# Performance work log

Hardware: AMD Instinct MI355X
Metric: run time of the kernel (lower is better)

## Reference

```python
import jax, jax.numpy as jnp
import numpy as np

EMBED_DIM = 1024
NUM_HEADS = 16
HEAD_DIM = EMBED_DIM // NUM_HEADS
EPS = 1e-5


def setup_inputs() -> dict:
    key = jax.random.key(0)
    ks = jax.random.split(key, 7)
    B, S, D = 4, 2048, EMBED_DIM
    s = 1.0 / np.sqrt(D)
    return {
        "x": jax.random.normal(ks[0], (B, S, D), dtype=jnp.float32),
        "W_qkv": jax.random.uniform(ks[1], (D, 3 * D), jnp.float32, -s, s),
        "b_qkv": jax.random.uniform(ks[2], (3 * D,), jnp.float32, -s, s),
        "W_out": jax.random.uniform(ks[3], (D, D), jnp.float32, -s, s),
        "b_out": jax.random.uniform(ks[4], (D,), jnp.float32, -s, s),
        "gamma": jnp.ones((D,), jnp.float32),
        "beta": jnp.zeros((D,), jnp.float32),
    }


def _layer_norm(y, gamma, beta):
    mu = jnp.mean(y, axis=-1, keepdims=True)
    var = jnp.mean(jnp.square(y - mu), axis=-1, keepdims=True)
    return (y - mu) * jax.lax.rsqrt(var + EPS) * gamma + beta


def reference(x, W_qkv, b_qkv, W_out, b_out, gamma, beta):
    B, S, D = x.shape
    H, Hd = NUM_HEADS, HEAD_DIM
    qkv = x @ W_qkv + b_qkv                       # [B,S,3D]
    q, k, v = jnp.split(qkv, 3, axis=-1)
    q = q.reshape(B, S, H, Hd).transpose(0, 2, 1, 3)  # [B,H,S,Hd]
    k = k.reshape(B, S, H, Hd).transpose(0, 2, 1, 3)
    v = v.reshape(B, S, H, Hd).transpose(0, 2, 1, 3)
    scale = 1.0 / np.sqrt(Hd)
    scores = jnp.einsum("bhsd,bhtd->bhst", q, k) * scale  # [B,H,S,S]
    attn = jax.nn.softmax(scores, axis=-1)
    ctx = jnp.einsum("bhst,bhtd->bhsd", attn, v)  # [B,H,S,Hd]
    ctx = ctx.transpose(0, 2, 1, 3).reshape(B, S, D)
    out = ctx @ W_out + b_out
    return _layer_norm(out + x, gamma, beta)
```

## Files before the change

### kernel.cpp

```cpp
#include <hip/hip_runtime.h>
#include <stdint.h>
#include <stddef.h>


#define SEQ    2048
#define DMODEL 1024
#define NHEAD  16
#define HDIM   64

typedef __attribute__((ext_vector_type(4))) float f32x4;
typedef __attribute__((ext_vector_type(16))) float f32x16;
typedef __attribute__((ext_vector_type(8))) short bf16x8;
typedef __attribute__((ext_vector_type(2))) unsigned uint2v;

static __device__ __forceinline__ unsigned short f2b(float f) {
  union { float f; unsigned u; } c; c.f = f;
  unsigned r = c.u + 0x7FFFu + ((c.u >> 16) & 1u);
  return (unsigned short)(r >> 16);
}
static __device__ __forceinline__ unsigned pkbf(float lo, float hi_) {
  unsigned r;
  asm("v_cvt_pk_bf16_f32 %0, %1, %2" : "=v"(r) : "v"(lo), "v"(hi_));
  return r;
}
static __device__ __forceinline__ float exp2v(float x) {
  return __builtin_amdgcn_exp2f(x);
}
static __device__ __forceinline__ uint2v swap32(unsigned a, unsigned b) {
  return __builtin_amdgcn_permlane32_swap(a, b, false, false);
}
static __device__ __forceinline__ void gl_lds16(const void* g, void* l) {
  __builtin_amdgcn_global_load_lds((const __attribute__((address_space(1))) void*)g,
                                   (__attribute__((address_space(3))) void*)l, 16, 0, 0);
}
static __device__ __forceinline__ int swz(int row, int col) {
  return (row * 64 + col) ^ ((row & 7) << 3);
}

__global__ __launch_bounds__(256) void k_prep(const float* __restrict__ Wqkv,
                                              const float* __restrict__ Wout,
                                              const float* __restrict__ X,
                                              unsigned short* __restrict__ wqkvT,
                                              unsigned short* __restrict__ woutT,
                                              unsigned short* __restrict__ Xb) {
  __shared__ unsigned short tile[32][33];
  const int bid = blockIdx.x;
  const int t = threadIdx.x;
  if (bid < 4096) {
    const float* in; unsigned short* out; int C, bx, by;
    if (bid < 3072) { in = Wqkv; out = wqkvT; C = 3072; bx = bid % 96; by = bid / 96; }
    else { int b2 = bid - 3072; in = Wout; out = woutT; C = 1024; bx = b2 & 31; by = b2 >> 5; }
    const int R = 1024;
    const int c0 = bx * 32, r0 = by * 32;
    const int tx = t & 31, ty = t >> 5;
#pragma unroll
    for (int j = 0; j < 4; j++) {
      int rr = ty + j * 8;
      tile[rr][tx] = f2b(in[(size_t)(r0 + rr) * C + c0 + tx]);
    }
    __syncthreads();
#pragma unroll
    for (int j = 0; j < 4; j++) {
      int rr = ty + j * 8;
      out[(size_t)(c0 + rr) * R + r0 + tx] = tile[tx][rr];
    }
  } else {
    const size_t i = ((size_t)(bid - 4096) * 256 + t) * 8;
    f32x4 a = *(const f32x4*)&X[i];
    f32x4 b = *(const f32x4*)&X[i + 4];
    bf16x8 o;
    o[0] = (short)f2b(a[0]); o[1] = (short)f2b(a[1]);
    o[2] = (short)f2b(a[2]); o[3] = (short)f2b(a[3]);
    o[4] = (short)f2b(b[0]); o[5] = (short)f2b(b[1]);
    o[6] = (short)f2b(b[2]); o[7] = (short)f2b(b[3]);
    *(bf16x8*)&Xb[i] = o;
  }
}

__global__ __launch_bounds__(256) void k_gemm_qkv(const unsigned short* __restrict__ X,
                                                  const unsigned short* __restrict__ WT,
                                                  const float* __restrict__ bias,
                                                  unsigned short* __restrict__ qb,
                                                  unsigned short* __restrict__ kb,
                                                  unsigned short* __restrict__ vt) {
  __shared__ __align__(16) unsigned short As[128 * 32];
  __shared__ __align__(16) unsigned short Bs[128 * 32];
  const int t = threadIdx.x;
  const int w = t >> 6, l = t & 63, g = l >> 4, r = l & 15;
  const int wr = w >> 1, wc = w & 1;
  const int bm = blockIdx.x * 128;
  const int bn = blockIdx.y * 128;

  f32x4 acc[4][4];
#pragma unroll
  for (int a = 0; a < 4; a++)
#pragma unroll
    for (int b = 0; b < 4; b++) acc[a][b] = f32x4{0.f, 0.f, 0.f, 0.f};

  for (int k0 = 0; k0 < DMODEL; k0 += 32) {
    __syncthreads();
#pragma unroll
    for (int j = 0; j < 2; j++) {
      int idx = t + j * 256;
      int row = idx >> 2, kc = idx & 3;
      gl_lds16(X + (size_t)(bm + row) * DMODEL + k0 + kc * 8, (char*)As + idx * 16);
      gl_lds16(WT + (size_t)(bn + row) * DMODEL + k0 + kc * 8, (char*)Bs + idx * 16);
    }
    __syncthreads();
    bf16x8 af[4], bf[4];
#pragma unroll
    for (int mf = 0; mf < 4; mf++)
      af[mf] = *(const bf16x8*)&As[(wr * 64 + mf * 16 + r) * 32 + g * 8];
#pragma unroll
    for (int nf = 0; nf < 4; nf++)
      bf[nf] = *(const bf16x8*)&Bs[(wc * 64 + nf * 16 + r) * 32 + g * 8];
#pragma unroll
    for (int mf = 0; mf < 4; mf++)
#pragma unroll
      for (int nf = 0; nf < 4; nf++)
        acc[mf][nf] = __builtin_amdgcn_mfma_f32_16x16x32_bf16(af[mf], bf[nf], acc[mf][nf], 0, 0, 0);
  }

  if (blockIdx.y >= 16) {
    __syncthreads();
    const int bi = bm >> 11, sbase = bm & 2047;
    const int h  = ((bn - 2048) >> 6) + wc;
    const int bh = bi * NHEAD + h;
    unsigned short* Ls = (w < 2) ? (As + w * 2048) : (Bs + (w - 2) * 2048);
#pragma unroll
    for (int p = 0; p < 2; p++) {
#pragma unroll
      for (int nfp = 0; nfp < 2; nfp++)
#pragma unroll
        for (int mf = 0; mf < 4; mf++)
#pragma unroll
          for (int i = 0; i < 4; i++) {
            const int nf = 2 * p + nfp;
            const int dd = nfp * 16 + r;
            const int ss = mf * 16 + g * 4 + i;
            float v = acc[mf][nf][i] + bias[bn + wc * 64 + nf * 16 + r];
            Ls[dd * 64 + (((ss >> 3) ^ (dd & 7)) * 8) + (ss & 7)] = f2b(v);
          }
#pragma unroll
      for (int j = 0; j < 4; j++) {
        const int dd = l >> 1;
        const int ch = (l & 1) * 4 + j;
        bf16x8 ov = *(const bf16x8*)&Ls[dd * 64 + ((ch ^ (dd & 7)) * 8)];
        *(bf16x8*)&vt[((size_t)bh * HDIM + 32 * p + dd) * SEQ + sbase + wr * 64 + ch * 8] = ov;
      }
    }
  } else {
#pragma unroll
    for (int mf = 0; mf < 4; mf++)
#pragma unroll
      for (int nf = 0; nf < 4; nf++)
#pragma unroll
        for (int i = 0; i < 4; i++) {
          int m = bm + wr * 64 + mf * 16 + g * 4 + i;
          int n = bn + wc * 64 + nf * 16 + r;
          float v = acc[mf][nf][i] + bias[n];
          int part = n >> 10, rem = n & 1023, h = rem >> 6, d = rem & 63;
          int bi = m >> 11, s = m & 2047;
          int bh = bi * NHEAD + h;
          if (part == 0)      qb[((size_t)bh * SEQ + s) * HDIM + d] = f2b(v * 0.18033688f);
          else                kb[((size_t)bh * SEQ + s) * HDIM + d] = f2b(v);
        }
  }
}

__global__ __launch_bounds__(512) void k_attn(const unsigned short* __restrict__ qb,
                                              const unsigned short* __restrict__ kb,
                                              const unsigned short* __restrict__ vt,
                                              unsigned short* __restrict__ ctx) {
  __shared__ __align__(16) unsigned short Qs[256 * 64];
  __shared__ __align__(16) unsigned short K0[64 * 64];
  __shared__ __align__(16) unsigned short K1[64 * 64];
  __shared__ __align__(16) unsigned short V0[64 * 64];
  __shared__ __align__(16) unsigned short V1[64 * 64];
  const int t = threadIdx.x;
  const int w = t >> 6, l = t & 63;
  const int ql = l & 31, hi = l >> 5;
  const int bid = blockIdx.x;
  const int xcd = bid & 7;
  const int j_  = bid >> 3;
  const int bh  = xcd * 8 + (j_ >> 3);
  const int q0  = (j_ & 7) * 256;
  const size_t qoff = ((size_t)bh * SEQ + q0) * HDIM;

#pragma unroll
  for (int j = 0; j < 4; j++) {
    int idx = t + j * 512;
    int row = idx >> 3, s = idx & 7;
    gl_lds16(qb + qoff + (size_t)row * 64 + (s ^ (row & 7)) * 8, (char*)Qs + idx * 16);
  }
  {
    int row = t >> 3, s = t & 7;
    gl_lds16(kb + ((size_t)bh * SEQ + row) * HDIM + (s ^ (row & 7)) * 8, (char*)K0 + t * 16);
    gl_lds16(vt + ((size_t)bh * HDIM + row) * SEQ + (s ^ (row & 7)) * 8, (char*)V0 + t * 16);
  }
  asm volatile("s_waitcnt vmcnt(2)" ::: "memory");
  __builtin_amdgcn_sched_barrier(0);
  __builtin_amdgcn_s_barrier();

  bf16x8 qf[4];
#pragma unroll
  for (int ds = 0; ds < 4; ds++)
    qf[ds] = *(const bf16x8*)&Qs[swz(w * 32 + ql, ds * 16 + hi * 8)];
  asm volatile("s_waitcnt lgkmcnt(0)" ::: "memory");

  bf16x8 ones;
#pragma unroll
  for (int i = 0; i < 8; i++) ones[i] = (short)0x3F80;

  f32x16 acc_o[2];
  f32x16 acc_l;
#pragma unroll
  for (int db = 0; db < 2; db++)
#pragma unroll
    for (int i = 0; i < 16; i++) acc_o[db][i] = 0.f;
#pragma unroll
  for (int i = 0; i < 16; i++) acc_l[i] = 0.f;

  for (int it = 0; it < SEQ / 64; ++it) {
    const int b = it & 1;
    if (it + 1 < SEQ / 64) {
      const int kt = (it + 1) * 64;
      unsigned short* Kd = b ? K0 : K1;
      unsigned short* Vd = b ? V0 : V1;
      {
        int row = t >> 3, s = t & 7;
        gl_lds16(kb + ((size_t)bh * SEQ + kt + row) * HDIM + (s ^ (row & 7)) * 8,
                 (char*)Kd + t * 16);
        gl_lds16(vt + ((size_t)bh * HDIM + row) * SEQ + kt + (s ^ (row & 7)) * 8,
                 (char*)Vd + t * 16);
      }
      asm volatile("s_waitcnt vmcnt(2)" ::: "memory");
    } else {
      asm volatile("s_waitcnt vmcnt(0)" ::: "memory");
    }
    __builtin_amdgcn_sched_barrier(0);
    __builtin_amdgcn_s_barrier();

    const unsigned short* Kb = b ? K1 : K0;
    const unsigned short* Vb = b ? V1 : V0;

    bf16x8 kf[2][4];
#pragma unroll
    for (int kb2 = 0; kb2 < 2; kb2++)
#pragma unroll
      for (int ds = 0; ds < 4; ds++)
        kf[kb2][ds] = *(const bf16x8*)&Kb[swz(kb2 * 32 + ql, ds * 16 + hi * 8)];

    f32x16 accs[2];
#pragma unroll
    for (int kb2 = 0; kb2 < 2; kb2++)
#pragma unroll
      for (int i = 0; i < 16; i++) accs[kb2][i] = 0.f;
    __builtin_amdgcn_s_setprio(1);
#pragma unroll
    for (int ds = 0; ds < 4; ds++)
#pragma unroll
      for (int kb2 = 0; kb2 < 2; kb2++)
        accs[kb2] = __builtin_amdgcn_mfma_f32_32x32x16_bf16(kf[kb2][ds], qf[ds], accs[kb2], 0, 0, 0);
    __builtin_amdgcn_s_setprio(0);

#pragma unroll
    for (int kb2 = 0; kb2 < 2; kb2++)
#pragma unroll
      for (int i = 0; i < 16; i++) accs[kb2][i] = exp2v(accs[kb2][i]);

    bf16x8 pa[4];
#pragma unroll
    for (int ks = 0; ks < 4; ks++) {
      const int kb2 = ks >> 1, rb = (ks & 1) * 8;
      unsigned wA0 = pkbf(accs[kb2][rb + 0], accs[kb2][rb + 1]);
      unsigned wA1 = pkbf(accs[kb2][rb + 2], accs[kb2][rb + 3]);
      unsigned wB0 = pkbf(accs[kb2][rb + 4], accs[kb2][rb + 5]);
      unsigned wB1 = pkbf(accs[kb2][rb + 6], accs[kb2][rb + 7]);
      uint2v s0 = swap32(wB0, wA0);
      uint2v s1 = swap32(wB1, wA1);
      union { bf16x8 v; unsigned u[4]; } fr;
      fr.u[0] = s0[1]; fr.u[1] = s1[1]; fr.u[2] = s0[0]; fr.u[3] = s1[0];
      pa[ks] = fr.v;
    }

    bf16x8 vf[2][4];
#pragma unroll
    for (int db = 0; db < 2; db++)
#pragma unroll
      for (int ks = 0; ks < 4; ks++)
        vf[db][ks] = *(const bf16x8*)&Vb[swz(db * 32 + ql, ks * 16 + hi * 8)];

    __builtin_amdgcn_s_setprio(1);
#pragma unroll
    for (int ks = 0; ks < 4; ks++) {
#pragma unroll
      for (int db = 0; db < 2; db++)
        acc_o[db] = __builtin_amdgcn_mfma_f32_32x32x16_bf16(vf[db][ks], pa[ks], acc_o[db], 0, 0, 0);
      acc_l = __builtin_amdgcn_mfma_f32_32x32x16_bf16(ones, pa[ks], acc_l, 0, 0, 0);
    }
    __builtin_amdgcn_s_setprio(0);

    __builtin_amdgcn_s_barrier();
  }

  const int bi = bh >> 4, h = bh & 15;
  const float rl = 1.f / acc_l[0];
  unsigned short* Ls = Qs + w * 2048;
#pragma unroll
  for (int db = 0; db < 2; db++)
#pragma unroll
    for (int j = 0; j < 8; j++) {
      const int d0 = db * 32 + (j & 1) * 2 + (j >> 1) * 8 + hi * 4;
      *(unsigned*)&Ls[(ql * 64 + d0) ^ ((ql & 7) << 3)] =
          pkbf(acc_o[db][2 * j] * rl, acc_o[db][2 * j + 1] * rl);
    }
#pragma unroll
  for (int rq = 0; rq < 4; rq++) {
    const int q = rq * 8 + (l >> 3);
    const int c8 = l & 7;
    bf16x8 ov = *(const bf16x8*)&Ls[(q * 64 + c8 * 8) ^ ((q & 7) << 3)];
    *(bf16x8*)&ctx[((size_t)bi * SEQ + q0 + w * 32 + q) * DMODEL + h * 64 + c8 * 8] = ov;
  }
}

__global__ __launch_bounds__(256) void k_gemm_out(const unsigned short* __restrict__ A,
                                                  const unsigned short* __restrict__ WT,
                                                  const float* __restrict__ bias,
                                                  const float* __restrict__ X,
                                                  float* __restrict__ Y) {
  __shared__ __align__(16) unsigned short As[128 * 32];
  __shared__ __align__(16) unsigned short Bs[128 * 32];
  const int t = threadIdx.x;
  const int w = t >> 6, l = t & 63, g = l >> 4, r = l & 15;
  const int wr = w >> 1, wc = w & 1;
  const int bm = blockIdx.x * 128;
  const int bn = blockIdx.y * 128;

  f32x4 acc[4][4];
#pragma unroll
  for (int a = 0; a < 4; a++)
#pragma unroll
    for (int b = 0; b < 4; b++) acc[a][b] = f32x4{0.f, 0.f, 0.f, 0.f};

  for (int k0 = 0; k0 < DMODEL; k0 += 32) {
    __syncthreads();
#pragma unroll
    for (int j = 0; j < 2; j++) {
      int idx = t + j * 256;
      int row = idx >> 2, kc = idx & 3;
      gl_lds16(A + (size_t)(bm + row) * DMODEL + k0 + kc * 8, (char*)As + idx * 16);
      gl_lds16(WT + (size_t)(bn + row) * DMODEL + k0 + kc * 8, (char*)Bs + idx * 16);
    }
    __syncthreads();
    bf16x8 af[4], bf[4];
#pragma unroll
    for (int mf = 0; mf < 4; mf++)
      af[mf] = *(const bf16x8*)&As[(wr * 64 + mf * 16 + r) * 32 + g * 8];
#pragma unroll
    for (int nf = 0; nf < 4; nf++)
      bf[nf] = *(const bf16x8*)&Bs[(wc * 64 + nf * 16 + r) * 32 + g * 8];
#pragma unroll
    for (int mf = 0; mf < 4; mf++)
#pragma unroll
      for (int nf = 0; nf < 4; nf++)
        acc[mf][nf] = __builtin_amdgcn_mfma_f32_16x16x32_bf16(af[mf], bf[nf], acc[mf][nf], 0, 0, 0);
  }

#pragma unroll
  for (int mf = 0; mf < 4; mf++)
#pragma unroll
    for (int nf = 0; nf < 4; nf++)
#pragma unroll
      for (int i = 0; i < 4; i++) {
        int m = bm + wr * 64 + mf * 16 + g * 4 + i;
        int n = bn + wc * 64 + nf * 16 + r;
        float v = acc[mf][nf][i] + bias[n] + X[(size_t)m * DMODEL + n];
        Y[(size_t)m * DMODEL + n] = v;
      }
}

__global__ __launch_bounds__(256) void k_ln(const float* __restrict__ Y,
                                            const float* __restrict__ gamma,
                                            const float* __restrict__ beta,
                                            float* __restrict__ out) {
  const int row = blockIdx.x, t = threadIdx.x;
  const float* y = Y + (size_t)row * DMODEL;
  f32x4 v = *(const f32x4*)&y[t * 4];
  float s = v[0] + v[1] + v[2] + v[3];
  float q = v[0] * v[0] + v[1] * v[1] + v[2] * v[2] + v[3] * v[3];
#pragma unroll
  for (int m = 1; m < 64; m <<= 1) { s += __shfl_xor(s, m); q += __shfl_xor(q, m); }
  __shared__ float ss[4], sq[4];
  const int w = t >> 6, l = t & 63;
  if (l == 0) { ss[w] = s; sq[w] = q; }
  __syncthreads();
  s = ss[0] + ss[1] + ss[2] + ss[3];
  q = sq[0] + sq[1] + sq[2] + sq[3];
  const float mu = s * (1.f / DMODEL);
  const float var = q * (1.f / DMODEL) - mu * mu;
  const float rs = rsqrtf(var + 1e-5f);
  f32x4 o;
#pragma unroll
  for (int j = 0; j < 4; j++)
    o[j] = (v[j] - mu) * rs * gamma[t * 4 + j] + beta[t * 4 + j];
  *(f32x4*)&out[(size_t)row * DMODEL + t * 4] = o;
}

extern "C" void kernel_launch(void* const* d_in, const int* in_sizes, int n_in,
                              void* d_out, int out_size, void* d_ws, size_t ws_size,
                              hipStream_t stream) {
  const float* X     = (const float*)d_in[0];
  const float* Wqkv  = (const float*)d_in[1];
  const float* bqkv  = (const float*)d_in[2];
  const float* Wout  = (const float*)d_in[3];
  const float* bout  = (const float*)d_in[4];
  const float* gamma = (const float*)d_in[5];
  const float* beta  = (const float*)d_in[6];

  char* ws = (char*)d_ws;
  unsigned short* wqkvT = (unsigned short*)(ws);
  unsigned short* woutT = (unsigned short*)(ws + 6291456);
  unsigned short* Xb    = (unsigned short*)(ws + 8388608);
  unsigned short* ctx   = (unsigned short*)(ws + 8388608);
  unsigned short* qb    = (unsigned short*)(ws + 25165824);
  unsigned short* kb    = (unsigned short*)(ws + 41943040);
  unsigned short* vt    = (unsigned short*)(ws + 58720256);
  float*          Yf    = (float*)d_out;

  k_prep<<<dim3(8192, 1, 1), dim3(256, 1, 1), 0, stream>>>(Wqkv, Wout, X, wqkvT, woutT, Xb);
  k_gemm_qkv<<<dim3(64, 24, 1), dim3(256, 1, 1), 0, stream>>>(Xb, wqkvT, bqkv, qb, kb, vt);
  k_attn<<<dim3(512, 1, 1), dim3(512, 1, 1), 0, stream>>>(qb, kb, vt, ctx);
  k_gemm_out<<<dim3(64, 8, 1), dim3(256, 1, 1), 0, stream>>>(ctx, woutT, bout, X, Yf);
  k_ln<<<dim3(8192, 1, 1), dim3(256, 1, 1), 0, stream>>>(Yf, gamma, beta, (float*)d_out);
}
```

Measured before the change: 208.5 us.

## Software-pipeline QK^T one tile ahead and replace ones-MFMA row sum with lane reduction

Restructures the attention loop so the QK^T MFMAs for the next key tile are issued before the exp/pack/PV work of the current tile, with K loaded two tiles ahead and V one tile ahead. Scores alternate between two accumulator sets across a manually unrolled pair of iterations. The softmax denominator is now a register sum plus a permlane32 swap instead of an extra MFMA against a ones vector. This removes a quarter of the PV MFMA work and overlaps matrix and transcendental work, at the cost of more live registers and fp32 rather than bf16-rounded denominators.

New measurement: 209.5 us. Within noise of the previous version (+0.5%).

```diff
diff --git a/kernel.cpp b/kernel.cpp
--- a/kernel.cpp
+++ b/kernel.cpp
@@ -28,6 +28,12 @@
 }
 static __device__ __forceinline__ uint2v swap32(unsigned a, unsigned b) {
   return __builtin_amdgcn_permlane32_swap(a, b, false, false);
+}
+static __device__ __forceinline__ float xchg_sum(float v) {
+  union { float f; unsigned u; } c; c.f = v;
+  uint2v p = swap32(c.u, c.u);
+  union { unsigned u; float f; } x, y; x.u = p[0]; y.u = p[1];
+  return x.f + y.f;
 }
 static __device__ __forceinline__ void gl_lds16(const void* g, void* l) {
   __builtin_amdgcn_global_load_lds((const __attribute__((address_space(1))) void*)g,
@@ -165,6 +171,82 @@
           if (part == 0)      qb[((size_t)bh * SEQ + s) * HDIM + d] = f2b(v * 0.18033688f);
           else                kb[((size_t)bh * SEQ + s) * HDIM + d] = f2b(v);
         }
+  }
+}
+
+static __device__ __forceinline__ void attn_iter(
+    int it, int t, int ql, int hi, int bh,
+    const unsigned short* __restrict__ kb, const unsigned short* __restrict__ vt,
+    unsigned short* K0, unsigned short* K1, unsigned short* V0, unsigned short* V1,
+    const bf16x8 (&qf)[4], f32x16 (&cur)[2], f32x16 (&nxt)[2],
+    f32x16 (&acc_o)[2], float& l_run) {
+  asm volatile("s_waitcnt vmcnt(0)" ::: "memory");
+  __builtin_amdgcn_sched_barrier(0);
+  __builtin_amdgcn_s_barrier();
+  if (it + 2 < SEQ / 64) {
+    int row = t >> 3, s = t & 7;
+    gl_lds16(kb + ((size_t)bh * SEQ + (it + 2) * 64 + row) * HDIM + (s ^ (row & 7)) * 8,
+             (char*)((it & 1) ? K1 : K0) + t * 16);
+  }
+  if (it + 1 < SEQ / 64) {
+    int row = t >> 3, s = t & 7;
+    gl_lds16(vt + ((size_t)bh * HDIM + row) * SEQ + (it + 1) * 64 + (s ^ (row & 7)) * 8,
+             (char*)(((it + 1) & 1) ? V1 : V0) + t * 16);
+  }
+  if (it + 1 < SEQ / 64) {
+    const unsigned short* Kc = ((it + 1) & 1) ? K1 : K0;
+#pragma unroll
+    for (int kb2 = 0; kb2 < 2; kb2++) {
+      bf16x8 kf[4];
+#pragma unroll
+      for (int ds = 0; ds < 4; ds++)
+        kf[ds] = *(const bf16x8*)&Kc[swz(kb2 * 32 + ql, ds * 16 + hi * 8)];
+#pragma unroll
+      for (int i = 0; i < 16; i++) nxt[kb2][i] = 0.f;
+      __builtin_amdgcn_s_setprio(1);
+#pragma unroll
+      for (int ds = 0; ds < 4; ds++)
+        nxt[kb2] = __builtin_amdgcn_mfma_f32_32x32x16_bf16(kf[ds], qf[ds], nxt[kb2], 0, 0, 0);
+      __builtin_amdgcn_s_setprio(0);
+    }
+  }
+#pragma unroll
+  for (int kb2 = 0; kb2 < 2; kb2++)
+#pragma unroll
+    for (int i = 0; i < 16; i++) cur[kb2][i] = exp2v(cur[kb2][i]);
+  float s8[8];
+#pragma unroll
+  for (int i = 0; i < 8; i++)
+    s8[i] = (cur[0][i] + cur[0][i + 8]) + (cur[1][i] + cur[1][i + 8]);
+  float sum = ((s8[0] + s8[1]) + (s8[2] + s8[3])) + ((s8[4] + s8[5]) + (s8[6] + s8[7]));
+  sum = xchg_sum(sum);
+  l_run += sum;
+  bf16x8 pa[4];
+#pragma unroll
+  for (int ks = 0; ks < 4; ks++) {
+    const int kb2 = ks >> 1, rb = (ks & 1) * 8;
+    unsigned wA0 = pkbf(cur[kb2][rb + 0], cur[kb2][rb + 1]);
+    unsigned wA1 = pkbf(cur[kb2][rb + 2], cur[kb2][rb + 3]);
+    unsigned wB0 = pkbf(cur[kb2][rb + 4], cur[kb2][rb + 5]);
+    unsigned wB1 = pkbf(cur[kb2][rb + 6], cur[kb2][rb + 7]);
+    uint2v s0 = swap32(wB0, wA0);
+    uint2v s1 = swap32(wB1, wA1);
+    union { bf16x8 v; unsigned u[4]; } fr;
+    fr.u[0] = s0[1]; fr.u[1] = s1[1]; fr.u[2] = s0[0]; fr.u[3] = s1[0];
+    pa[ks] = fr.v;
+  }
+  const unsigned short* Vc = (it & 1) ? V1 : V0;
+#pragma unroll
+  for (int db = 0; db < 2; db++) {
+    bf16x8 vf[4];
+#pragma unroll
+    for (int ks = 0; ks < 4; ks++)
+      vf[ks] = *(const bf16x8*)&Vc[swz(db * 32 + ql, ks * 16 + hi * 8)];
+    __builtin_amdgcn_s_setprio(1);
+#pragma unroll
+    for (int ks = 0; ks < 4; ks++)
+      acc_o[db] = __builtin_amdgcn_mfma_f32_32x32x16_bf16(vf[ks], pa[ks], acc_o[db], 0, 0, 0);
+    __builtin_amdgcn_s_setprio(0);
   }
 }
 
@@ -197,115 +279,51 @@
     int row = t >> 3, s = t & 7;
     gl_lds16(kb + ((size_t)bh * SEQ + row) * HDIM + (s ^ (row & 7)) * 8, (char*)K0 + t * 16);
     gl_lds16(vt + ((size_t)bh * HDIM + row) * SEQ + (s ^ (row & 7)) * 8, (char*)V0 + t * 16);
-  }
+    gl_lds16(kb + ((size_t)bh * SEQ + 64 + row) * HDIM + (s ^ (row & 7)) * 8, (char*)K1 + t * 16);
+  }
+  asm volatile("s_waitcnt vmcnt(3)" ::: "memory");
+  __builtin_amdgcn_sched_barrier(0);
+  __builtin_amdgcn_s_barrier();
+
+  bf16x8 qf[4];
+#pragma unroll
+  for (int ds = 0; ds < 4; ds++)
+    qf[ds] = *(const bf16x8*)&Qs[swz(w * 32 + ql, ds * 16 + hi * 8)];
+  asm volatile("s_waitcnt lgkmcnt(0)" ::: "memory");
+
   asm volatile("s_waitcnt vmcnt(2)" ::: "memory");
   __builtin_amdgcn_sched_barrier(0);
   __builtin_amdgcn_s_barrier();
 
-  bf16x8 qf[4];
-#pragma unroll
-  for (int ds = 0; ds < 4; ds++)
-    qf[ds] = *(const bf16x8*)&Qs[swz(w * 32 + ql, ds * 16 + hi * 8)];
-  asm volatile("s_waitcnt lgkmcnt(0)" ::: "memory");
-
-  bf16x8 ones;
-#pragma unroll
-  for (int i = 0; i < 8; i++) ones[i] = (short)0x3F80;
-
+  f32x16 accsA[2], accsB[2];
   f32x16 acc_o[2];
-  f32x16 acc_l;
+  float l_run = 0.f;
 #pragma unroll
   for (int db = 0; db < 2; db++)
 #pragma unroll
     for (int i = 0; i < 16; i++) acc_o[db][i] = 0.f;
 #pragma unroll
-  for (int i = 0; i < 16; i++) acc_l[i] = 0.f;
-
-  for (int it = 0; it < SEQ / 64; ++it) {
-    const int b = it & 1;
-    if (it + 1 < SEQ / 64) {
-      const int kt = (it + 1) * 64;
-      unsigned short* Kd = b ? K0 : K1;
-      unsigned short* Vd = b ? V0 : V1;
-      {
-        int row = t >> 3, s = t & 7;
-        gl_lds16(kb + ((size_t)bh * SEQ + kt + row) * HDIM + (s ^ (row & 7)) * 8,
-                 (char*)Kd + t * 16);
-        gl_lds16(vt + ((size_t)bh * HDIM + row) * SEQ + kt + (s ^ (row & 7)) * 8,
-                 (char*)Vd + t * 16);
-      }
-      asm volatile("s_waitcnt vmcnt(2)" ::: "memory");
-    } else {
-      asm volatile("s_waitcnt vmcnt(0)" ::: "memory");
-    }
-    __builtin_amdgcn_sched_barrier(0);
-    __builtin_amdgcn_s_barrier();
-
-    const unsigned short* Kb = b ? K1 : K0;
-    const unsigned short* Vb = b ? V1 : V0;
-
-    bf16x8 kf[2][4];
-#pragma unroll
-    for (int kb2 = 0; kb2 < 2; kb2++)
-#pragma unroll
-      for (int ds = 0; ds < 4; ds++)
-        kf[kb2][ds] = *(const bf16x8*)&Kb[swz(kb2 * 32 + ql, ds * 16 + hi * 8)];
-
-    f32x16 accs[2];
-#pragma unroll
-    for (int kb2 = 0; kb2 < 2; kb2++)
-#pragma unroll
-      for (int i = 0; i < 16; i++) accs[kb2][i] = 0.f;
+  for (int kb2 = 0; kb2 < 2; kb2++) {
+    bf16x8 kf[4];
+#pragma unroll
+    for (int ds = 0; ds < 4; ds++)
+      kf[ds] = *(const bf16x8*)&K0[swz(kb2 * 32 + ql, ds * 16 + hi * 8)];
+#pragma unroll
+    for (int i = 0; i < 16; i++) accsA[kb2][i] = 0.f;
     __builtin_amdgcn_s_setprio(1);
 #pragma unroll
     for (int ds = 0; ds < 4; ds++)
-#pragma unroll
-      for (int kb2 = 0; kb2 < 2; kb2++)
-        accs[kb2] = __builtin_amdgcn_mfma_f32_32x32x16_bf16(kf[kb2][ds], qf[ds], accs[kb2], 0, 0, 0);
+      accsA[kb2] = __builtin_amdgcn_mfma_f32_32x32x16_bf16(kf[ds], qf[ds], accsA[kb2], 0, 0, 0);
     __builtin_amdgcn_s_setprio(0);
-
-#pragma unroll
-    for (int kb2 = 0; kb2 < 2; kb2++)
-#pragma unroll
-      for (int i = 0; i < 16; i++) accs[kb2][i] = exp2v(accs[kb2][i]);
-
-    bf16x8 pa[4];
-#pragma unroll
-    for (int ks = 0; ks < 4; ks++) {
-      const int kb2 = ks >> 1, rb = (ks & 1) * 8;
-      unsigned wA0 = pkbf(accs[kb2][rb + 0], accs[kb2][rb + 1]);
-      unsigned wA1 = pkbf(accs[kb2][rb + 2], accs[kb2][rb + 3]);
-      unsigned wB0 = pkbf(accs[kb2][rb + 4], accs[kb2][rb + 5]);
-      unsigned wB1 = pkbf(accs[kb2][rb + 6], accs[kb2][rb + 7]);
-      uint2v s0 = swap32(wB0, wA0);
-      uint2v s1 = swap32(wB1, wA1);
-      union { bf16x8 v; unsigned u[4]; } fr;
-      fr.u[0] = s0[1]; fr.u[1] = s1[1]; fr.u[2] = s0[0]; fr.u[3] = s1[0];
-      pa[ks] = fr.v;
-    }
-
-    bf16x8 vf[2][4];
-#pragma unroll
-    for (int db = 0; db < 2; db++)
-#pragma unroll
-      for (int ks = 0; ks < 4; ks++)
-        vf[db][ks] = *(const bf16x8*)&Vb[swz(db * 32 + ql, ks * 16 + hi * 8)];
-
-    __builtin_amdgcn_s_setprio(1);
-#pragma unroll
-    for (int ks = 0; ks < 4; ks++) {
-#pragma unroll
-      for (int db = 0; db < 2; db++)
-        acc_o[db] = __builtin_amdgcn_mfma_f32_32x32x16_bf16(vf[db][ks], pa[ks], acc_o[db], 0, 0, 0);
-      acc_l = __builtin_amdgcn_mfma_f32_32x32x16_bf16(ones, pa[ks], acc_l, 0, 0, 0);
-    }
-    __builtin_amdgcn_s_setprio(0);
-
-    __builtin_amdgcn_s_barrier();
+  }
+
+  for (int it2 = 0; it2 < SEQ / 64; it2 += 2) {
+    attn_iter(it2,     t, ql, hi, bh, kb, vt, K0, K1, V0, V1, qf, accsA, accsB, acc_o, l_run);
+    attn_iter(it2 + 1, t, ql, hi, bh, kb, vt, K0, K1, V0, V1, qf, accsB, accsA, acc_o, l_run);
   }
 
   const int bi = bh >> 4, h = bh & 15;
-  const float rl = 1.f / acc_l[0];
+  const float rl = 1.f / l_run;
   unsigned short* Ls = Qs + w * 2048;
 #pragma unroll
   for (int db = 0; db < 2; db++)
```

## Replace ones-MFMA row sum with VALU reduction and alias Q staging LDS

Applied to the files above, without the earlier changes.

The attention kernel no longer computes the softmax denominator with an extra MFMA against a ones vector. Each lane now sums its exponentiated scores in scalar adds and combines the two half-waves with a permlane32 swap. The Q staging buffer is also aliased onto the K/V double buffers, which shrinks LDS per block (possibly allowing more blocks per CU) but adds a barrier and serializes the Q load before the first K/V load. Accumulating in fp32 VALU instead of from bf16-rounded P slightly changes the normalization numerics, and it trades matrix-core work for extra vector ALU adds.

After: 204.1 us. -2.1%, faster.

```diff
diff --git a/kernel.cpp b/kernel.cpp
--- a/kernel.cpp
+++ b/kernel.cpp
@@ -28,6 +28,12 @@
 }
 static __device__ __forceinline__ uint2v swap32(unsigned a, unsigned b) {
   return __builtin_amdgcn_permlane32_swap(a, b, false, false);
+}
+static __device__ __forceinline__ float xchg_sum(float v) {
+  union { float f; unsigned u; } c; c.f = v;
+  uint2v p = swap32(c.u, c.u);
+  union { unsigned u; float f; } x, y; x.u = p[0]; y.u = p[1];
+  return x.f + y.f;
 }
 static __device__ __forceinline__ void gl_lds16(const void* g, void* l) {
   __builtin_amdgcn_global_load_lds((const __attribute__((address_space(1))) void*)g,
@@ -172,11 +178,11 @@
                                               const unsigned short* __restrict__ kb,
                                               const unsigned short* __restrict__ vt,
                                               unsigned short* __restrict__ ctx) {
-  __shared__ __align__(16) unsigned short Qs[256 * 64];
-  __shared__ __align__(16) unsigned short K0[64 * 64];
-  __shared__ __align__(16) unsigned short K1[64 * 64];
-  __shared__ __align__(16) unsigned short V0[64 * 64];
-  __shared__ __align__(16) unsigned short V1[64 * 64];
+  __shared__ __align__(16) unsigned short S[16384];
+  unsigned short* K0 = S;
+  unsigned short* K1 = S + 4096;
+  unsigned short* V0 = S + 8192;
+  unsigned short* V1 = S + 12288;
   const int t = threadIdx.x;
   const int w = t >> 6, l = t & 63;
   const int ql = l & 31, hi = l >> 5;
@@ -191,35 +197,32 @@
   for (int j = 0; j < 4; j++) {
     int idx = t + j * 512;
     int row = idx >> 3, s = idx & 7;
-    gl_lds16(qb + qoff + (size_t)row * 64 + (s ^ (row & 7)) * 8, (char*)Qs + idx * 16);
-  }
+    gl_lds16(qb + qoff + (size_t)row * 64 + (s ^ (row & 7)) * 8, (char*)S + idx * 16);
+  }
+  asm volatile("s_waitcnt vmcnt(0)" ::: "memory");
+  __builtin_amdgcn_sched_barrier(0);
+  __builtin_amdgcn_s_barrier();
+
+  bf16x8 qf[4];
+#pragma unroll
+  for (int ds = 0; ds < 4; ds++)
+    qf[ds] = *(const bf16x8*)&S[swz(w * 32 + ql, ds * 16 + hi * 8)];
+  asm volatile("s_waitcnt lgkmcnt(0)" ::: "memory");
+  __builtin_amdgcn_sched_barrier(0);
+  __builtin_amdgcn_s_barrier();
+
   {
     int row = t >> 3, s = t & 7;
     gl_lds16(kb + ((size_t)bh * SEQ + row) * HDIM + (s ^ (row & 7)) * 8, (char*)K0 + t * 16);
     gl_lds16(vt + ((size_t)bh * HDIM + row) * SEQ + (s ^ (row & 7)) * 8, (char*)V0 + t * 16);
   }
-  asm volatile("s_waitcnt vmcnt(2)" ::: "memory");
-  __builtin_amdgcn_sched_barrier(0);
-  __builtin_amdgcn_s_barrier();
-
-  bf16x8 qf[4];
-#pragma unroll
-  for (int ds = 0; ds < 4; ds++)
-    qf[ds] = *(const bf16x8*)&Qs[swz(w * 32 + ql, ds * 16 + hi * 8)];
-  asm volatile("s_waitcnt lgkmcnt(0)" ::: "memory");
-
-  bf16x8 ones;
-#pragma unroll
-  for (int i = 0; i < 8; i++) ones[i] = (short)0x3F80;
 
   f32x16 acc_o[2];
-  f32x16 acc_l;
+  float l_run = 0.f;
 #pragma unroll
   for (int db = 0; db < 2; db++)
 #pragma unroll
     for (int i = 0; i < 16; i++) acc_o[db][i] = 0.f;
-#pragma unroll
-  for (int i = 0; i < 16; i++) acc_l[i] = 0.f;
 
   for (int it = 0; it < SEQ / 64; ++it) {
     const int b = it & 1;
@@ -268,6 +271,13 @@
     for (int kb2 = 0; kb2 < 2; kb2++)
 #pragma unroll
       for (int i = 0; i < 16; i++) accs[kb2][i] = exp2v(accs[kb2][i]);
+    float s8[8];
+#pragma unroll
+    for (int i = 0; i < 8; i++)
+      s8[i] = (accs[0][i] + accs[0][i + 8]) + (accs[1][i] + accs[1][i + 8]);
+    float sum = ((s8[0] + s8[1]) + (s8[2] + s8[3])) + ((s8[4] + s8[5]) + (s8[6] + s8[7]));
+    sum = xchg_sum(sum);
+    l_run += sum;
 
     bf16x8 pa[4];
 #pragma unroll
@@ -293,20 +303,18 @@
 
     __builtin_amdgcn_s_setprio(1);
 #pragma unroll
-    for (int ks = 0; ks < 4; ks++) {
+    for (int ks = 0; ks < 4; ks++)
 #pragma unroll
       for (int db = 0; db < 2; db++)
         acc_o[db] = __builtin_amdgcn_mfma_f32_32x32x16_bf16(vf[db][ks], pa[ks], acc_o[db], 0, 0, 0);
-      acc_l = __builtin_amdgcn_mfma_f32_32x32x16_bf16(ones, pa[ks], acc_l, 0, 0, 0);
-    }
     __builtin_amdgcn_s_setprio(0);
 
     __builtin_amdgcn_s_barrier();
   }
 
   const int bi = bh >> 4, h = bh & 15;
-  const float rl = 1.f / acc_l[0];
-  unsigned short* Ls = Qs + w * 2048;
+  const float rl = 1.f / l_run;
+  unsigned short* Ls = S + w * 2048;
 #pragma unroll
   for (int db = 0; db < 2; db++)
 #pragma unroll
```
